# Kernel tuning notes

Hardware: AMD Instinct MI355X
Metric: run time of the kernel (lower is better)

Reference implementation:

```python
import jax, jax.numpy as jnp
import numpy as np

D_MODEL = 64
HEADS = 8
LEVELS = 5
POINTS = 4
DH = D_MODEL // HEADS
EPS = 1e-5


def _layernorm(x, g, b):
    m = x.mean(-1, keepdims=True)
    v = ((x - m) ** 2).mean(-1, keepdims=True)
    return (x - m) / jnp.sqrt(v + EPS) * g + b


def _bilinear_sample(v, lx, ly, Hl, Wl):
    # v: (B, heads, Hl, Wl, dh); lx, ly: (B, Nq, heads, P) normalized in ~[0,1]
    # matches F.grid_sample(align_corners=False, padding_mode='zeros')
    x = lx * Wl - 0.5
    y = ly * Hl - 0.5
    x0 = jnp.floor(x)
    y0 = jnp.floor(y)
    wx = x - x0
    wy = y - y0
    x0i = x0.astype(jnp.int32)
    y0i = y0.astype(jnp.int32)
    B, heads = v.shape[0], v.shape[1]
    bidx = jnp.arange(B)[:, None, None, None]
    hidx = jnp.arange(heads)[None, None, :, None]

    def gather(yi, xi):
        valid = (xi >= 0) & (xi < Wl) & (yi >= 0) & (yi < Hl)
        xc = jnp.clip(xi, 0, Wl - 1)
        yc = jnp.clip(yi, 0, Hl - 1)
        g = v[bidx, hidx, yc, xc]  # (B, Nq, heads, P, dh)
        return g * valid[..., None].astype(v.dtype)

    return (gather(y0i, x0i) * ((1 - wx) * (1 - wy))[..., None]
            + gather(y0i, x0i + 1) * (wx * (1 - wy))[..., None]
            + gather(y0i + 1, x0i) * ((1 - wx) * wy)[..., None]
            + gather(y0i + 1, x0i + 1) * (wx * wy)[..., None])


def setup_inputs() -> dict:
    key = jax.random.key(0)
    ks = jax.random.split(key, 24)
    B, NQ = 2, 20000
    ss = np.array([[184, 184], [92, 92], [46, 46], [23, 23], [12, 12]], dtype=np.int64)
    areas = ss[:, 0] * ss[:, 1]
    lsi = np.concatenate([[0], np.cumsum(areas)[:-1]]).astype(np.int64)
    LIN = int(areas.sum())  # 45109
    s = 0.02
    inp = {
        'q_feat': jax.random.normal(ks[0], (B, NQ, D_MODEL), jnp.float32),
        'dense_voxel_flatten': jax.random.normal(ks[1], (B, LIN, D_MODEL), jnp.float32),
        'reference_points': jax.random.uniform(ks[2], (B, NQ, 2), jnp.float32),
        'q_pos': jax.random.normal(ks[3], (B, NQ, D_MODEL), jnp.float32),
        'spatial_shapes': ss,
        'level_start_index': lsi,
        'Wv': jax.random.normal(ks[4], (D_MODEL, D_MODEL), jnp.float32) * s,
        'bv': jnp.zeros((D_MODEL,), jnp.float32),
        'Wo': jax.random.normal(ks[5], (D_MODEL, HEADS * LEVELS * POINTS * 2), jnp.float32) * s,
        'bo': jax.random.normal(ks[6], (HEADS * LEVELS * POINTS * 2,), jnp.float32),
        'Wa': jax.random.normal(ks[7], (D_MODEL, HEADS * LEVELS * POINTS), jnp.float32) * s,
        'ba': jnp.zeros((HEADS * LEVELS * POINTS,), jnp.float32),
        'Wout': jax.random.normal(ks[8], (D_MODEL, D_MODEL), jnp.float32) * s,
        'bout': jnp.zeros((D_MODEL,), jnp.float32),
        'g1': jnp.ones((D_MODEL,), jnp.float32),
        'b1': jnp.zeros((D_MODEL,), jnp.float32),
        'W1': jax.random.normal(ks[9], (D_MODEL, 1024), jnp.float32) * s,
        'bff1': jnp.zeros((1024,), jnp.float32),
        'W2': jax.random.normal(ks[10], (1024, D_MODEL), jnp.float32) * s,
        'bff2': jnp.zeros((D_MODEL,), jnp.float32),
        'g2': jnp.ones((D_MODEL,), jnp.float32),
        'b2': jnp.zeros((D_MODEL,), jnp.float32),
    }
    return inp


def reference(q_feat, dense_voxel_flatten, reference_points, q_pos,
              spatial_shapes, level_start_index,
              Wv, bv, Wo, bo, Wa, ba, Wout, bout,
              g1, b1, W1, bff1, W2, bff2, g2, b2):
    B, NQ, _ = q_feat.shape
    q = q_feat + q_pos  # with_pos_embed
    value = (dense_voxel_flatten @ Wv + bv).reshape(B, -1, HEADS, DH)
    off = (q @ Wo + bo).reshape(B, NQ, HEADS, LEVELS, POINTS, 2)
    aw = jax.nn.softmax((q @ Wa + ba).reshape(B, NQ, HEADS, LEVELS * POINTS), axis=-1)
    aw = aw.reshape(B, NQ, HEADS, LEVELS, POINTS)
    # offset normalizer is (W, H) per level
    ssn = np.asarray(spatial_shapes)
    normalizer = jnp.asarray(ssn[:, ::-1].copy(), q.dtype)  # (L, 2)
    loc = reference_points[:, :, None, None, None, :] + off / normalizer[None, None, None, :, None, :]
    out = jnp.zeros((B, NQ, HEADS, DH), q.dtype)
    for l in range(LEVELS):
        Hl, Wl = int(ssn[l, 0]), int(ssn[l, 1])
        st = int(np.asarray(level_start_index)[l])
        vl = value[:, st:st + Hl * Wl].reshape(B, Hl, Wl, HEADS, DH).transpose(0, 3, 1, 2, 4)
        sampled = _bilinear_sample(vl, loc[:, :, :, l, :, 0], loc[:, :, :, l, :, 1], Hl, Wl)
        out = out + jnp.einsum('bnhpd,bnhp->bnhd', sampled, aw[:, :, :, l])
    attn_out = out.reshape(B, NQ, D_MODEL) @ Wout + bout
    x = _layernorm(q_feat + attn_out, g1, b1)  # residual + norm1 (dropout=0)
    ffn = jax.nn.relu(x @ W1 + bff1) @ W2 + bff2
    return _layernorm(x + ffn, g2, b2)
```

## Files before the change

kernel.cpp:

```cpp
#include <hip/hip_runtime.h>
#include <hip/hip_bf16.h>

#define NB 2
#define NQ 20000
#define DM 64
#define NH 8
#define NL 5
#define NP 4
#define LIN 45109
#define FFN 1024

typedef __attribute__((ext_vector_type(8))) short short8;
typedef __attribute__((ext_vector_type(4))) float f32x4;

__device__ __forceinline__ float b2f(const __hip_bfloat16 h) { return __bfloat162float(h); }
__device__ __forceinline__ float lo16f(unsigned u) { return __uint_as_float(u << 16); }
__device__ __forceinline__ float hi16f(unsigned u) { return __uint_as_float(u & 0xffff0000u); }
__device__ __forceinline__ unsigned f2bf_bits(float x) {
    unsigned u = __float_as_uint(x);
    return (u + 0x7FFFu + ((u >> 16) & 1u)) >> 16;
}

__global__ void __launch_bounds__(256)
val_proj_kernel(const float* __restrict__ dvf,
                const float* __restrict__ Wv,
                const float* __restrict__ bv,
                __hip_bfloat16* __restrict__ valA,
                __hip_bfloat16* __restrict__ valB,
                int rows) {
    __shared__ __align__(16) __hip_bfloat16 wvp[8][64][8];
    __shared__ __align__(16) __hip_bfloat16 ar[64][72];
    __shared__ __align__(16) float bvs[64];

    const int tid = threadIdx.x;
    const int lane = tid & 63;
    const int w = tid >> 6;
    const int m16 = lane & 15, qd = lane >> 4;
    const int row0 = blockIdx.x * 64;

    for (int idx = tid; idx < 4096; idx += 256) {
        const int j = idx & 7;
        const int l = (idx >> 3) & 63;
        const int seg = idx >> 9;
        const int nt = seg >> 1, kc = seg & 1;
        const int n = nt * 16 + (l & 15);
        const int k = kc * 32 + (l >> 4) * 8 + j;
        wvp[seg][l][j] = __float2bfloat16(Wv[k * 64 + n]);
    }
    if (tid < 64) bvs[tid] = bv[tid];

    {
        const int r = w * 16 + m16;
        const int grow = row0 + r;
        const int c0 = qd * 16;
        __hip_bfloat16* dst = &ar[r][c0];
        if (grow < rows) {
            const float4* src = (const float4*)&dvf[(size_t)grow * DM + c0];
#pragma unroll
            for (int t = 0; t < 4; t++) {
                const float4 v = src[t];
                dst[t * 4 + 0] = __float2bfloat16(v.x);
                dst[t * 4 + 1] = __float2bfloat16(v.y);
                dst[t * 4 + 2] = __float2bfloat16(v.z);
                dst[t * 4 + 3] = __float2bfloat16(v.w);
            }
        } else {
#pragma unroll
            for (int t = 0; t < 16; t++) dst[t] = __float2bfloat16(0.f);
        }
    }
    __syncthreads();

    f32x4 acc[4];
#pragma unroll
    for (int nt = 0; nt < 4; nt++) acc[nt] = (f32x4){0.f, 0.f, 0.f, 0.f};
#pragma unroll
    for (int kc = 0; kc < 2; kc++) {
        const short8 a = *(const short8*)&ar[w * 16 + m16][kc * 32 + qd * 8];
#pragma unroll
        for (int nt = 0; nt < 4; nt++) {
            const short8 b = *(const short8*)&wvp[nt * 2 + kc][lane][0];
            acc[nt] = __builtin_amdgcn_mfma_f32_16x16x32_bf16(a, b, acc[nt], 0, 0, 0);
        }
    }

#pragma unroll
    for (int r = 0; r < 4; r++) {
        const int gr = row0 + w * 16 + qd * 4 + r;
        if (gr < rows) {
            __hip_bfloat16* dst = (gr < LIN) ? (valA + (size_t)gr * DM)
                                             : (valB + (size_t)(gr - LIN) * DM);
#pragma unroll
            for (int nt = 0; nt < 4; nt++) {
                const int col = nt * 16 + m16;
                dst[col] = __float2bfloat16(acc[nt][r] + bvs[col]);
            }
        }
    }
}

__global__ void pack_kernel(const float* __restrict__ W1, const float* __restrict__ W2,
                            const float* __restrict__ Wo, const float* __restrict__ Wa,
                            const float* __restrict__ Wout,
                            __hip_bfloat16* __restrict__ W1p, __hip_bfloat16* __restrict__ W2p,
                            __hip_bfloat16* __restrict__ Woap, __hip_bfloat16* __restrict__ Woutp) {
    const int t = blockIdx.x * 256 + threadIdx.x;
    const int lane = t & 63;
    const int m = lane & 15, qd = lane >> 4;
    const int seg = t >> 6;
    if (seg < 128) {
        const int nt = seg >> 1, kc = seg & 1;
        const int n = nt * 16 + m, kb = kc * 32 + qd * 8;
        __hip_bfloat16* dst = W1p + ((size_t)seg * 64 + lane) * 8;
#pragma unroll
        for (int j = 0; j < 8; j++) dst[j] = __float2bfloat16(W1[(size_t)(kb + j) * FFN + n]);
    } else if (seg < 256) {
        const int sl = seg - 128;
        const int nt = sl >> 5, kc = sl & 31;
        const int n = nt * 16 + m, kb = kc * 32 + qd * 8;
        __hip_bfloat16* dst = W2p + ((size_t)sl * 64 + lane) * 8;
#pragma unroll
        for (int j = 0; j < 8; j++) dst[j] = __float2bfloat16(W2[(size_t)(kb + j) * DM + n]);
    } else if (seg < 316) {
        const int sl = seg - 256;
        const int nt = sl >> 1, kc = sl & 1;
        const int n = nt * 16 + m, kb = kc * 32 + qd * 8;
        __hip_bfloat16* dst = Woap + ((size_t)sl * 64 + lane) * 8;
#pragma unroll
        for (int j = 0; j < 8; j++) {
            const int k = kb + j;
            const float v = (n < 320) ? Wo[(size_t)k * 320 + n] : Wa[(size_t)k * 160 + (n - 320)];
            dst[j] = __float2bfloat16(v);
        }
    } else if (seg < 324) {
        const int sl = seg - 316;
        const int nt = sl >> 1, kc = sl & 1;
        const int n = nt * 16 + m, kb = kc * 32 + qd * 8;
        __hip_bfloat16* dst = Woutp + ((size_t)sl * 64 + lane) * 8;
#pragma unroll
        for (int j = 0; j < 8; j++) dst[j] = __float2bfloat16(Wout[(size_t)(kb + j) * DM + n]);
    }
}

__global__ void __launch_bounds__(256)
attn4_kernel(const float* __restrict__ q_feat,
             const float* __restrict__ ref_pts,
             const float* __restrict__ q_pos,
             const __hip_bfloat16* __restrict__ Woap,
             const float* __restrict__ bo, const float* __restrict__ ba,
             const __hip_bfloat16* __restrict__ Woutp, const float* __restrict__ bout,
             const float* __restrict__ g1, const float* __restrict__ b1,
             const __hip_bfloat16* __restrict__ valA,
             const __hip_bfloat16* __restrict__ valB,
             int qoff,
             float* __restrict__ xout) {
    __shared__ __align__(16) __hip_bfloat16 qb[16][72];
    __shared__ __align__(16) float offs[4][321];
    __shared__ __align__(16) float aws[4][161];
    __shared__ __align__(16) float refs[4][2];
    __shared__ __align__(16) int   dco[640][4];
    __shared__ __align__(16) uint2 dwp[640];
    __shared__ __align__(16) float xs4[4][64];

    const int tid = threadIdx.x;
    const int lane = tid & 63;
    const int w = tid >> 6;
    const int m16 = lane & 15, qd = lane >> 4;
    const int q0 = qoff + blockIdx.x * 4;
    const int qi = q0 + w;

    const int sz[NL]  = {184, 92, 46, 23, 12};
    const int lsi[NL] = {0, 33856, 42320, 44436, 44965};

    const __hip_bfloat16* valp = (q0 >= NQ) ? valB : valA;

    const float qf = q_feat[(size_t)qi * DM + lane];
    const float qp = q_pos[(size_t)qi * DM + lane];
    qb[w][lane] = __float2bfloat16(qf + qp);
    for (int idx = tid; idx < 12 * 64; idx += 256)
        qb[4 + (idx >> 6)][idx & 63] = __float2bfloat16(0.f);
    if (tid < 8) refs[tid >> 1][tid & 1] = ref_pts[(size_t)(q0 + (tid >> 1)) * 2 + (tid & 1)];
    __syncthreads();

    for (int nt = w; nt < 30; nt += 4) {
        f32x4 acc = {0.f, 0.f, 0.f, 0.f};
#pragma unroll
        for (int kc = 0; kc < 2; kc++) {
            const short8 a = *(const short8*)&qb[m16][kc * 32 + qd * 8];
            const short8 b = *(const short8*)(Woap + ((size_t)(nt * 2 + kc) * 64 + lane) * 8);
            acc = __builtin_amdgcn_mfma_f32_16x16x32_bf16(a, b, acc, 0, 0, 0);
        }
        if (qd == 0) {
            const int n = nt * 16 + m16;
            if (n < 320) {
                const float bn = bo[n];
#pragma unroll
                for (int r = 0; r < 4; r++) offs[r][n] = acc[r] + bn;
            } else {
                const float bn = ba[n - 320];
#pragma unroll
                for (int r = 0; r < 4; r++) aws[r][n - 320] = acc[r] + bn;
            }
        }
    }
    __syncthreads();

    if (tid < 32) {
        const int q = tid >> 3, h = tid & 7;
        float* p = &aws[q][h * 20];
        float mx = p[0];
        for (int j = 1; j < 20; j++) mx = fmaxf(mx, p[j]);
        float s = 0.f;
        for (int j = 0; j < 20; j++) { const float e = expf(p[j] - mx); p[j] = e; s += e; }
        const float inv = 1.f / s;
        for (int j = 0; j < 20; j++) p[j] *= inv;
    }
    __syncthreads();

    for (int s = tid; s < 640; s += 256) {
        const int h = s & 7;
        const int t2 = s >> 3;
        const int p = t2 & 3;
        const int t3 = t2 >> 2;
        const int l = t3 % 5;
        const int q = t3 / 5;
        const int Wl = sz[l];
        const float Wf = (float)Wl;
        const int st = lsi[l];
        const int c = ((h * 5 + l) * 4 + p) * 2;
        const float ox = offs[q][c], oy = offs[q][c + 1];
        const float fx = (refs[q][0] + ox / Wf) * Wf - 0.5f;
        const float fy = (refs[q][1] + oy / Wf) * Wf - 0.5f;
        const float x0f = floorf(fx), y0f = floorf(fy);
        const float wx = fx - x0f, wy = fy - y0f;
        const int x0 = (int)x0f, y0 = (int)y0f;
        const float aV = aws[q][h * 20 + l * 4 + p];
        const bool xin0 = (x0 >= 0) & (x0 < Wl), xin1 = (x0 + 1 >= 0) & (x0 + 1 < Wl);
        const bool yin0 = (y0 >= 0) & (y0 < Wl), yin1 = (y0 + 1 >= 0) & (y0 + 1 < Wl);
        int4 co;
        float w00 = 0.f, w10 = 0.f, w01 = 0.f, w11 = 0.f;
        co.x = (xin0 && yin0) ? (st + y0 * Wl + x0) * DM : 0;
        if (xin0 && yin0) w00 = (1.f - wx) * (1.f - wy) * aV;
        co.y = (xin1 && yin0) ? (st + y0 * Wl + x0 + 1) * DM : 0;
        if (xin1 && yin0) w10 = wx * (1.f - wy) * aV;
        co.z = (xin0 && yin1) ? (st + (y0 + 1) * Wl + x0) * DM : 0;
        if (xin0 && yin1) w01 = (1.f - wx) * wy * aV;
        co.w = (xin1 && yin1) ? (st + (y0 + 1) * Wl + x0 + 1) * DM : 0;
        if (xin1 && yin1) w11 = wx * wy * aV;
        *(int4*)dco[s] = co;
        uint2 dw;
        dw.x = f2bf_bits(w00) | (f2bf_bits(w10) << 16);
        dw.y = f2bf_bits(w01) | (f2bf_bits(w11) << 16);
        dwp[s] = dw;
    }
    __syncthreads();

    {
        const int h = lane >> 3;
        const __hip_bfloat16* vbase = valp + lane;
        float acc = 0.f;
#pragma unroll
        for (int l = 0; l < NL; l++) {
#pragma unroll
            for (int p = 0; p < NP; p++) {
                const int idx = ((w * 5 + l) * 4 + p) * 8 + h;
                const int4 co = *(const int4*)dco[idx];
                const uint2 dw = dwp[idx];
                acc = fmaf(lo16f(dw.x), b2f(vbase[co.x]), acc);
                acc = fmaf(hi16f(dw.x), b2f(vbase[co.y]), acc);
                acc = fmaf(lo16f(dw.y), b2f(vbase[co.z]), acc);
                acc = fmaf(hi16f(dw.y), b2f(vbase[co.w]), acc);
            }
        }
        qb[w][lane] = __float2bfloat16(acc);
    }
    __syncthreads();

    {
        f32x4 acc = {0.f, 0.f, 0.f, 0.f};
#pragma unroll
        for (int kc = 0; kc < 2; kc++) {
            const short8 a = *(const short8*)&qb[m16][kc * 32 + qd * 8];
            const short8 b = *(const short8*)(Woutp + ((size_t)(w * 2 + kc) * 64 + lane) * 8);
            acc = __builtin_amdgcn_mfma_f32_16x16x32_bf16(a, b, acc, 0, 0, 0);
        }
        if (qd == 0) {
            const int n = w * 16 + m16;
            const float bn = bout[n];
#pragma unroll
            for (int r = 0; r < 4; r++) xs4[r][n] = acc[r] + bn;
        }
    }
    __syncthreads();

    {
        const float xpre = qf + xs4[w][lane];
        float s = xpre, s2 = xpre * xpre;
#pragma unroll
        for (int o = 32; o >= 1; o >>= 1) {
            s += __shfl_xor(s, o, 64);
            s2 += __shfl_xor(s2, o, 64);
        }
        const float mean = s * (1.f / 64.f);
        const float var = s2 * (1.f / 64.f) - mean * mean;
        const float xn = (xpre - mean) * rsqrtf(var + 1e-5f);
        xout[(size_t)qi * DM + lane] = xn * g1[lane] + b1[lane];
    }
}

__global__ void __launch_bounds__(256)
ffn_kernel(const __hip_bfloat16* __restrict__ W1p, const float* __restrict__ bff1,
           const __hip_bfloat16* __restrict__ W2p, const float* __restrict__ bff2,
           const float* __restrict__ g2, const float* __restrict__ b2,
           float* __restrict__ io) {
    __shared__ __align__(16) __hip_bfloat16 xb[32][72];
    __shared__ __align__(16) __hip_bfloat16 hb[32][264];
    __shared__ __align__(16) float yr[32][64];

    const int tid = threadIdx.x;
    const int lane = tid & 63;
    const int w = tid >> 6;
    const int m16 = lane & 15, qd = lane >> 4;
    const int q0 = blockIdx.x * 32;

    {
        const int q = tid >> 3, i = tid & 7;
        const float4 v0 = *(const float4*)&io[(size_t)(q0 + q) * DM + i * 8];
        const float4 v1 = *(const float4*)&io[(size_t)(q0 + q) * DM + i * 8 + 4];
        __hip_bfloat16* xp = &xb[q][i * 8];
        xp[0] = __float2bfloat16(v0.x); xp[1] = __float2bfloat16(v0.y);
        xp[2] = __float2bfloat16(v0.z); xp[3] = __float2bfloat16(v0.w);
        xp[4] = __float2bfloat16(v1.x); xp[5] = __float2bfloat16(v1.y);
        xp[6] = __float2bfloat16(v1.z); xp[7] = __float2bfloat16(v1.w);
    }
    __syncthreads();

    f32x4 yacc[2];
    yacc[0] = (f32x4){0.f, 0.f, 0.f, 0.f};
    yacc[1] = (f32x4){0.f, 0.f, 0.f, 0.f};

#pragma unroll
    for (int qtr = 0; qtr < 4; qtr++) {
#pragma unroll
        for (int ti = 0; ti < 4; ti++) {
            const int nt = qtr * 16 + w + ti * 4;
            f32x4 acc[2];
            acc[0] = (f32x4){0.f, 0.f, 0.f, 0.f};
            acc[1] = (f32x4){0.f, 0.f, 0.f, 0.f};
#pragma unroll
            for (int kc = 0; kc < 2; kc++) {
                const short8 b = *(const short8*)(W1p + ((size_t)(nt * 2 + kc) * 64 + lane) * 8);
#pragma unroll
                for (int mt = 0; mt < 2; mt++) {
                    const short8 a = *(const short8*)&xb[mt * 16 + m16][kc * 32 + qd * 8];
                    acc[mt] = __builtin_amdgcn_mfma_f32_16x16x32_bf16(a, b, acc[mt], 0, 0, 0);
                }
            }
            const int ncol = (nt - qtr * 16) * 16 + m16;
            const float bn = bff1[nt * 16 + m16];
#pragma unroll
            for (int mt = 0; mt < 2; mt++)
#pragma unroll
                for (int r = 0; r < 4; r++)
                    hb[mt * 16 + qd * 4 + r][ncol] = __float2bfloat16(fmaxf(acc[mt][r] + bn, 0.f));
        }
        __syncthreads();
#pragma unroll
        for (int kc2 = 0; kc2 < 8; kc2++) {
            const short8 b = *(const short8*)(W2p + ((size_t)(w * 32 + qtr * 8 + kc2) * 64 + lane) * 8);
#pragma unroll
            for (int mt = 0; mt < 2; mt++) {
                const short8 a = *(const short8*)&hb[mt * 16 + m16][kc2 * 32 + qd * 8];
                yacc[mt] = __builtin_amdgcn_mfma_f32_16x16x32_bf16(a, b, yacc[mt], 0, 0, 0);
            }
        }
        __syncthreads();
    }

    {
        const int n = w * 16 + m16;
        const float bn = bff2[n];
#pragma unroll
        for (int mt = 0; mt < 2; mt++)
#pragma unroll
            for (int r = 0; r < 4; r++) {
                const int mm = mt * 16 + qd * 4 + r;
                yr[mm][n] = yacc[mt][r] + bn;
            }
    }
    __syncthreads();

    {
        const int q = tid >> 3, i = tid & 7;
        const float4 x0 = *(const float4*)&io[(size_t)(q0 + q) * DM + i * 8];
        const float4 x1 = *(const float4*)&io[(size_t)(q0 + q) * DM + i * 8 + 4];
        float4 v0 = *(const float4*)&yr[q][i * 8];
        float4 v1 = *(const float4*)&yr[q][i * 8 + 4];
        v0.x += x0.x; v0.y += x0.y; v0.z += x0.z; v0.w += x0.w;
        v1.x += x1.x; v1.y += x1.y; v1.z += x1.z; v1.w += x1.w;
        float s = v0.x + v0.y + v0.z + v0.w + v1.x + v1.y + v1.z + v1.w;
        float s2 = v0.x * v0.x + v0.y * v0.y + v0.z * v0.z + v0.w * v0.w
                 + v1.x * v1.x + v1.y * v1.y + v1.z * v1.z + v1.w * v1.w;
#pragma unroll
        for (int o = 4; o >= 1; o >>= 1) { s += __shfl_xor(s, o, 64); s2 += __shfl_xor(s2, o, 64); }
        const float mean = s * (1.f / 64.f);
        const float var = s2 * (1.f / 64.f) - mean * mean;
        const float rstd = rsqrtf(var + 1e-5f);
        const float4 ga = *(const float4*)&g2[i * 8];
        const float4 gb = *(const float4*)&g2[i * 8 + 4];
        const float4 ba4 = *(const float4*)&b2[i * 8];
        const float4 bb4 = *(const float4*)&b2[i * 8 + 4];
        float4 o0, o1;
        o0.x = (v0.x - mean) * rstd * ga.x + ba4.x;
        o0.y = (v0.y - mean) * rstd * ga.y + ba4.y;
        o0.z = (v0.z - mean) * rstd * ga.z + ba4.z;
        o0.w = (v0.w - mean) * rstd * ga.w + ba4.w;
        o1.x = (v1.x - mean) * rstd * gb.x + bb4.x;
        o1.y = (v1.y - mean) * rstd * gb.y + bb4.y;
        o1.z = (v1.z - mean) * rstd * gb.z + bb4.z;
        o1.w = (v1.w - mean) * rstd * gb.w + bb4.w;
        *(float4*)&io[(size_t)(q0 + q) * DM + i * 8] = o0;
        *(float4*)&io[(size_t)(q0 + q) * DM + i * 8 + 4] = o1;
    }
}

extern "C" void kernel_launch(void* const* d_in, const int* in_sizes, int n_in,
                              void* d_out, int out_size, void* d_ws, size_t ws_size,
                              hipStream_t stream) {
    const int B0 = (in_sizes[4] >= 4096) ? 4 : 6;
    const float* q_feat = (const float*)d_in[0];
    const float* dvf    = (const float*)d_in[1];
    const float* refp   = (const float*)d_in[2];
    const float* q_pos  = (const float*)d_in[3];
    const float* Wv   = (const float*)d_in[B0 + 0];
    const float* bv   = (const float*)d_in[B0 + 1];
    const float* Wo   = (const float*)d_in[B0 + 2];
    const float* bo   = (const float*)d_in[B0 + 3];
    const float* Wa   = (const float*)d_in[B0 + 4];
    const float* ba   = (const float*)d_in[B0 + 5];
    const float* Wout = (const float*)d_in[B0 + 6];
    const float* bout = (const float*)d_in[B0 + 7];
    const float* g1   = (const float*)d_in[B0 + 8];
    const float* b1   = (const float*)d_in[B0 + 9];
    const float* W1   = (const float*)d_in[B0 + 10];
    const float* bff1 = (const float*)d_in[B0 + 11];
    const float* W2   = (const float*)d_in[B0 + 12];
    const float* bff2 = (const float*)d_in[B0 + 13];
    const float* g2   = (const float*)d_in[B0 + 14];
    const float* b2   = (const float*)d_in[B0 + 15];
    float* out = (float*)d_out;

    const size_t val_elems = (size_t)LIN * DM;
    const size_t pack_elems = (size_t)(128 + 128 + 60 + 8) * 64 * 8;
    const bool dbuf = ws_size >= (pack_elems + 2 * val_elems) * sizeof(__hip_bfloat16);

    __hip_bfloat16* W1p = (__hip_bfloat16*)d_ws;
    __hip_bfloat16* W2p = W1p + (size_t)128 * 64 * 8;
    __hip_bfloat16* Woap = W2p + (size_t)128 * 64 * 8;
    __hip_bfloat16* Woutp = Woap + (size_t)60 * 64 * 8;
    __hip_bfloat16* val0 = W1p + pack_elems;
    __hip_bfloat16* val1 = dbuf ? val0 + val_elems : val0;

    pack_kernel<<<81, 256, 0, stream>>>(W1, W2, Wo, Wa, Wout, W1p, W2p, Woap, Woutp);

    if (dbuf) {
        val_proj_kernel<<<(2 * LIN + 63) / 64, 256, 0, stream>>>(
            dvf, Wv, bv, val0, val1, 2 * LIN);
        attn4_kernel<<<(NB * NQ) / 4, 256, 0, stream>>>(
            q_feat, refp, q_pos, Woap, bo, ba, Woutp, bout, g1, b1,
            val0, val1, 0, out);
    } else {
        for (int b = 0; b < NB; b++) {
            val_proj_kernel<<<(LIN + 63) / 64, 256, 0, stream>>>(
                dvf + (size_t)b * val_elems, Wv, bv, val0, val0, LIN);
            attn4_kernel<<<NQ / 4, 256, 0, stream>>>(
                q_feat, refp, q_pos, Woap, bo, ba, Woutp, bout, g1, b1,
                val0, val0, b * NQ, out);
        }
    }
    ffn_kernel<<<(NB * NQ) / 32, 256, 0, stream>>>(W1p, bff1, W2p, bff2, g2, b2, out);
}
```

Baseline: 243.3 us.

## Store one base offset per sample, parallelize softmax, add occupancy hint

The four corner offsets stored per sample in shared memory are replaced by a single clamped base offset. The gather derives the other three corners by adding +DM and +row stride, relying on a zero-padded region after the value buffer so out-of-range reads stay safe. That padded region is cleared with a memset on every launch. The softmax moves from 32 serial threads to all 256 threads using 8-lane shuffle reductions. Launch bounds ask for 8 blocks per CU, and the sum now uses four independent accumulators for more ILP. One risk: clamped bases can read neighbouring batch or level data, which is only correct because those weights are zeroed, and out-of-bounds reads depend on the pad size being large enough.

```diff
diff --git a/kernel.cpp b/kernel.cpp
--- a/kernel.cpp
+++ b/kernel.cpp
@@ -142,7 +142,7 @@
     }
 }
 
-__global__ void __launch_bounds__(256)
+__global__ void __launch_bounds__(256, 8)
 attn4_kernel(const float* __restrict__ q_feat,
              const float* __restrict__ ref_pts,
              const float* __restrict__ q_pos,
@@ -158,7 +158,7 @@
     __shared__ __align__(16) float offs[4][321];
     __shared__ __align__(16) float aws[4][161];
     __shared__ __align__(16) float refs[4][2];
-    __shared__ __align__(16) int   dco[640][4];
+    __shared__ __align__(16) int   dbase[640];
     __shared__ __align__(16) uint2 dwp[640];
     __shared__ __align__(16) float xs4[4][64];
 
@@ -205,15 +205,27 @@
     }
     __syncthreads();
 
-    if (tid < 32) {
-        const int q = tid >> 3, h = tid & 7;
+    {
+        const int g = tid >> 3;
+        const int q = g >> 3, h = g & 7;
+        const int j = tid & 7;
         float* p = &aws[q][h * 20];
-        float mx = p[0];
-        for (int j = 1; j < 20; j++) mx = fmaxf(mx, p[j]);
-        float s = 0.f;
-        for (int j = 0; j < 20; j++) { const float e = expf(p[j] - mx); p[j] = e; s += e; }
+        const float v0 = p[j], v1 = p[j + 8];
+        const float v2 = (j < 4) ? p[j + 16] : -1e30f;
+        float mx = fmaxf(fmaxf(v0, v1), v2);
+        mx = fmaxf(mx, __shfl_xor(mx, 1, 8));
+        mx = fmaxf(mx, __shfl_xor(mx, 2, 8));
+        mx = fmaxf(mx, __shfl_xor(mx, 4, 8));
+        const float e0 = __expf(v0 - mx), e1 = __expf(v1 - mx);
+        const float e2 = (j < 4) ? __expf(v2 - mx) : 0.f;
+        float s = e0 + e1 + e2;
+        s += __shfl_xor(s, 1, 8);
+        s += __shfl_xor(s, 2, 8);
+        s += __shfl_xor(s, 4, 8);
         const float inv = 1.f / s;
-        for (int j = 0; j < 20; j++) p[j] *= inv;
+        p[j] = e0 * inv;
+        p[j + 8] = e1 * inv;
+        if (j < 4) p[j + 16] = e2 * inv;
     }
     __syncthreads();
 
@@ -228,26 +240,24 @@
         const float Wf = (float)Wl;
         const int st = lsi[l];
         const int c = ((h * 5 + l) * 4 + p) * 2;
-        const float ox = offs[q][c], oy = offs[q][c + 1];
-        const float fx = (refs[q][0] + ox / Wf) * Wf - 0.5f;
-        const float fy = (refs[q][1] + oy / Wf) * Wf - 0.5f;
+        const float fx = fmaf(refs[q][0], Wf, offs[q][c]) - 0.5f;
+        const float fy = fmaf(refs[q][1], Wf, offs[q][c + 1]) - 0.5f;
         const float x0f = floorf(fx), y0f = floorf(fy);
         const float wx = fx - x0f, wy = fy - y0f;
         const int x0 = (int)x0f, y0 = (int)y0f;
         const float aV = aws[q][h * 20 + l * 4 + p];
-        const bool xin0 = (x0 >= 0) & (x0 < Wl), xin1 = (x0 + 1 >= 0) & (x0 + 1 < Wl);
-        const bool yin0 = (y0 >= 0) & (y0 < Wl), yin1 = (y0 + 1 >= 0) & (y0 + 1 < Wl);
-        int4 co;
-        float w00 = 0.f, w10 = 0.f, w01 = 0.f, w11 = 0.f;
-        co.x = (xin0 && yin0) ? (st + y0 * Wl + x0) * DM : 0;
-        if (xin0 && yin0) w00 = (1.f - wx) * (1.f - wy) * aV;
-        co.y = (xin1 && yin0) ? (st + y0 * Wl + x0 + 1) * DM : 0;
-        if (xin1 && yin0) w10 = wx * (1.f - wy) * aV;
-        co.z = (xin0 && yin1) ? (st + (y0 + 1) * Wl + x0) * DM : 0;
-        if (xin0 && yin1) w01 = (1.f - wx) * wy * aV;
-        co.w = (xin1 && yin1) ? (st + (y0 + 1) * Wl + x0 + 1) * DM : 0;
-        if (xin1 && yin1) w11 = wx * wy * aV;
-        *(int4*)dco[s] = co;
+        const bool xin0 = (x0 >= 0) & (x0 < Wl);
+        const bool xin1 = (x0 >= -1) & (x0 < Wl - 1);
+        const bool yin0 = (y0 >= 0) & (y0 < Wl);
+        const bool yin1 = (y0 >= -1) & (y0 < Wl - 1);
+        const float w00 = (xin0 & yin0) ? (1.f - wx) * (1.f - wy) * aV : 0.f;
+        const float w10 = (xin1 & yin0) ? wx * (1.f - wy) * aV : 0.f;
+        const float w01 = (xin0 & yin1) ? (1.f - wx) * wy * aV : 0.f;
+        const float w11 = (xin1 & yin1) ? wx * wy * aV : 0.f;
+        int base = (st + y0 * Wl + x0) * DM;
+        base = base < -12160 ? -12160 : base;
+        base = base > LIN * DM ? LIN * DM : base;
+        dbase[s] = base;
         uint2 dw;
         dw.x = f2bf_bits(w00) | (f2bf_bits(w10) << 16);
         dw.y = f2bf_bits(w01) | (f2bf_bits(w11) << 16);
@@ -258,21 +268,24 @@
     {
         const int h = lane >> 3;
         const __hip_bfloat16* vbase = valp + lane;
-        float acc = 0.f;
+        float a0 = 0.f, a1 = 0.f, a2 = 0.f, a3 = 0.f;
+        const int wl64[NL] = {184 * DM, 92 * DM, 46 * DM, 23 * DM, 12 * DM};
 #pragma unroll
         for (int l = 0; l < NL; l++) {
 #pragma unroll
             for (int p = 0; p < NP; p++) {
                 const int idx = ((w * 5 + l) * 4 + p) * 8 + h;
-                const int4 co = *(const int4*)dco[idx];
+                const int base = dbase[idx];
                 const uint2 dw = dwp[idx];
-                acc = fmaf(lo16f(dw.x), b2f(vbase[co.x]), acc);
-                acc = fmaf(hi16f(dw.x), b2f(vbase[co.y]), acc);
-                acc = fmaf(lo16f(dw.y), b2f(vbase[co.z]), acc);
-                acc = fmaf(hi16f(dw.y), b2f(vbase[co.w]), acc);
-            }
-        }
-        qb[w][lane] = __float2bfloat16(acc);
+                const __hip_bfloat16* r0 = vbase + base;
+                const __hip_bfloat16* r1 = r0 + wl64[l];
+                a0 = fmaf(lo16f(dw.x), b2f(r0[0]), a0);
+                a1 = fmaf(hi16f(dw.x), b2f(r0[DM]), a1);
+                a2 = fmaf(lo16f(dw.y), b2f(r1[0]), a2);
+                a3 = fmaf(hi16f(dw.y), b2f(r1[DM]), a3);
+            }
+        }
+        qb[w][lane] = __float2bfloat16((a0 + a1) + (a2 + a3));
     }
     __syncthreads();
 
@@ -452,7 +465,8 @@
 
     const size_t val_elems = (size_t)LIN * DM;
     const size_t pack_elems = (size_t)(128 + 128 + 60 + 8) * 64 * 8;
-    const bool dbuf = ws_size >= (pack_elems + 2 * val_elems) * sizeof(__hip_bfloat16);
+    const size_t PAD_ELEMS = 12288;
+    const bool dbuf = ws_size >= (pack_elems + 2 * val_elems + PAD_ELEMS) * sizeof(__hip_bfloat16);
 
     __hip_bfloat16* W1p = (__hip_bfloat16*)d_ws;
     __hip_bfloat16* W2p = W1p + (size_t)128 * 64 * 8;
@@ -460,6 +474,9 @@
     __hip_bfloat16* Woutp = Woap + (size_t)60 * 64 * 8;
     __hip_bfloat16* val0 = W1p + pack_elems;
     __hip_bfloat16* val1 = dbuf ? val0 + val_elems : val0;
+
+    __hip_bfloat16* pad_ptr = val1 + val_elems;
+    hipMemsetAsync(pad_ptr, 0, PAD_ELEMS * sizeof(__hip_bfloat16), stream);
 
     pack_kernel<<<81, 256, 0, stream>>>(W1, W2, Wo, Wa, Wout, W1p, W2p, Woap, Woutp);
 
```

After: 265.4 us. +9.1%, slower.
